# Performance work log

Measured on AMD Instinct MI355X. Metric: run time of the kernel, lower is better.

The kernel has to match this reference:

```python
import jax, jax.numpy as jnp
import numpy as np

B, L, D = 4, 2048, 256
H = 8
HD = D // H  # head_dim = 32


def setup_inputs() -> dict:
    key = jax.random.key(0)
    k1, k2, k3, k4 = jax.random.split(key, 4)
    x = jax.random.normal(k1, (B, L, D), dtype=jnp.float32)
    attn_bias = jax.random.normal(k2, (1, 1, L, L), dtype=jnp.float32)
    # Linear weights (stored as [in, out]; bias=False in the module)
    Wqkv = jax.random.normal(k3, (D, 3 * D), dtype=jnp.float32) * (D ** -0.5)
    Wout = jax.random.normal(k4, (D, D), dtype=jnp.float32) * (D ** -0.5)
    return {"x": x, "attn_bias": attn_bias, "Wqkv": Wqkv, "Wout": Wout}


def reference(x, attn_bias, Wqkv, Wout):
    scale = HD ** -0.5
    qkv = x @ Wqkv                                  # [B, L, 3D]
    q, k, v = jnp.split(qkv, 3, axis=-1)            # each [B, L, D]
    # b l (h d) -> b h l d
    def split_heads(t):
        return t.reshape(B, L, H, HD).transpose(0, 2, 1, 3)
    q, k, v = split_heads(q), split_heads(k), split_heads(v)
    scores = jnp.einsum('bhid,bhjd->bhij', q, k) * scale  # [B, H, L, L]
    scores = scores + attn_bias
    attn = jax.nn.softmax(scores, axis=-1)
    out = jnp.einsum('bhij,bhjd->bhid', attn, v)    # [B, H, L, HD]
    out = out.transpose(0, 2, 1, 3).reshape(B, L, D)
    return out @ Wout
```

## Files before the change

kernel.cpp:

```cpp
#include <hip/hip_runtime.h>
#include <hip/hip_bf16.h>
#include <math.h>

#define B 4
#define L 2048
#define D 256
#define H 8
#define HD 32
#define KVB 64
#define SCALE 0.17677669529663687f
#define LOG2E 1.4426950408889634f
#define QSCL (SCALE * LOG2E)

typedef __attribute__((ext_vector_type(8))) short short8;
typedef __attribute__((ext_vector_type(4))) short short4v;
typedef __attribute__((ext_vector_type(4))) float f32x4;

__device__ inline short f2bf(float x) {
  union { float f; unsigned u; } c; c.f = x;
  unsigned r = (c.u + 0x7FFFu + ((c.u >> 16) & 1u)) >> 16;
  return (short)r;
}
__device__ inline float bf2f(short s) {
  union { unsigned u; float f; } c;
  c.u = ((unsigned)(unsigned short)s) << 16;
  return c.f;
}

#define GLOAD_LDS16(gp, lp)                                                  \
  __builtin_amdgcn_global_load_lds(                                          \
      (const __attribute__((address_space(1))) unsigned*)(const void*)(gp),  \
      (__attribute__((address_space(3))) unsigned*)(void*)(lp), 16, 0, 0)


__global__ __launch_bounds__(256) void prep_xb(const float* __restrict__ x,
                                               short* __restrict__ xb) {
  int i = (blockIdx.x * 256 + threadIdx.x) * 8;
  f32x4 a = *reinterpret_cast<const f32x4*>(x + i);
  f32x4 b = *reinterpret_cast<const f32x4*>(x + i + 4);
  short8 o;
#pragma unroll
  for (int j = 0; j < 4; ++j) { o[j] = f2bf(a[j]); o[4 + j] = f2bf(b[j]); }
  *reinterpret_cast<short8*>(xb + i) = o;
}

__global__ __launch_bounds__(256) void prep_bias(const float* __restrict__ bias,
                                                 short* __restrict__ bp) {
  int base = (blockIdx.x * 256 + threadIdx.x) * 8;
  int q = base >> 11;
  int rem = base & 2047;
  int kvt = rem >> 6;
  int wi = rem & 63;
  int g = wi >> 4;
  int c0 = (wi & 15) >> 2;
  const float* src = bias + (long)q * L + kvt * 64 + c0 * 16 + g * 4;
  f32x4 b0 = *reinterpret_cast<const f32x4*>(src);
  f32x4 b1 = *reinterpret_cast<const f32x4*>(src + 16);
  short8 o;
#pragma unroll
  for (int j = 0; j < 4; ++j) { o[j] = f2bf(b0[j]); o[4 + j] = f2bf(b1[j]); }
  *reinterpret_cast<short8*>(bp + base) = o;
}

__global__ __launch_bounds__(256) void prep_wt(const float* __restrict__ w,
                                               short* __restrict__ wt, int N) {
  __shared__ short tile[32][33];
  int k0 = blockIdx.x * 32;
  int n0 = blockIdx.y * 32;
  int tx = threadIdx.x & 31, ty = threadIdx.x >> 5;
#pragma unroll
  for (int i = 0; i < 32; i += 8)
    tile[ty + i][tx] = f2bf(w[(k0 + ty + i) * N + n0 + tx]);
  __syncthreads();
#pragma unroll
  for (int i = 0; i < 32; i += 8)
    wt[(n0 + ty + i) * 256 + k0 + tx] = tile[tx][ty + i];
}

__global__ __launch_bounds__(64) void qkv_gemm(const short* __restrict__ xb,
                                               const short* __restrict__ wt,
                                               short* __restrict__ qb,
                                               short* __restrict__ kb,
                                               short* __restrict__ vt) {
  int bid = blockIdx.x;
  int mt = bid / 12, nt = bid % 12;
  int m0 = mt * 64, n0 = nt * 64;
  int l = threadIdx.x, ra = l & 15, g = l >> 4;

  f32x4 acc[4][4] = {};
  for (int k0 = 0; k0 < 256; k0 += 32) {
    int kk = k0 + g * 8;
    short8 bfr[4], afr[4];
#pragma unroll
    for (int nf = 0; nf < 4; ++nf)
      bfr[nf] = *reinterpret_cast<const short8*>(&wt[(n0 + nf * 16 + ra) * 256 + kk]);
#pragma unroll
    for (int mf = 0; mf < 4; ++mf)
      afr[mf] = *reinterpret_cast<const short8*>(&xb[(m0 + mf * 16 + ra) * 256 + kk]);
#pragma unroll
    for (int mf = 0; mf < 4; ++mf)
#pragma unroll
      for (int nf = 0; nf < 4; ++nf)
        acc[mf][nf] = __builtin_amdgcn_mfma_f32_16x16x32_bf16(afr[mf], bfr[nf], acc[mf][nf], 0, 0, 0);
  }

  int sec = n0 >> 8;
  float scl = (sec == 0) ? QSCL : 1.0f;
#pragma unroll
  for (int nf = 0; nf < 4; ++nf) {
    int n = n0 + nf * 16 + ra;
    int c = n & 255;
    int h = c >> 5, d = c & 31;
#pragma unroll
    for (int mf = 0; mf < 4; ++mf) {
#pragma unroll
      for (int r = 0; r < 4; ++r) {
        int mm = m0 + mf * 16 + g * 4 + r;
        int b = mm >> 11, lpos = mm & 2047;
        short val = f2bf(acc[mf][nf][r] * scl);
        if (sec == 2) vt[((b * H + h) * HD + d) * L + lpos] = val;
        else {
          short* dst = (sec == 0) ? qb : kb;
          dst[((b * H + h) * L + lpos) * HD + d] = val;
        }
      }
    }
  }
}

__global__ __launch_bounds__(512, 4) void attn_fwd(const short* __restrict__ qb,
                                                   const short* __restrict__ kb,
                                                   const short* __restrict__ vt,
                                                   const short* __restrict__ bp,
                                                   short* __restrict__ ob) {
  __shared__ short kvlds[2][8][512];

  int wid = threadIdx.x >> 6;
  int l = threadIdx.x & 63;
  int ra = l & 15, g = l >> 4;
  bool oddg = (g & 1);
  int x = blockIdx.x & 7;
  int y = (blockIdx.x >> 3) & 3;
  int qblk = blockIdx.x >> 5;
  int bh = x * 4 + y;
  int q0 = qblk * 128 + wid * 16;

  const short* kbase = kb + bh * (L * HD);
  const short* vbase = vt + bh * (HD * L);
  const short* bpbase = bp + (q0 + ra) * L + g * 16;

  short8 bq = *reinterpret_cast<const short8*>(qb + (bh * L + q0 + ra) * HD + g * 8);

  const short* gsrc0;
  int gstep;
  if (wid < 4) { gsrc0 = kbase + (16 * wid + ra) * HD + g * 8; gstep = KVB * HD; }
  else {
    int j = wid - 4;
    gsrc0 = vbase + ((j >> 1) * 16 + ra) * L + (j & 1) * 32 + g * 8;
    gstep = KVB;
  }

  f32x4 o0 = {}, o1 = {}, zf = {};
  float mrun = -1e30f, lsum = 0.f;
  short8 bbX[2], bbY[2];

  auto STAGE = [&](int buf, int t) {
    GLOAD_LDS16(gsrc0 + (size_t)t * gstep, &kvlds[buf][wid][0]);
  };
  auto BLOAD = [&](short8 (&bb)[2], int t) {
    const short* p = bpbase + t * KVB;
    bb[0] = *reinterpret_cast<const short8*>(p);
    bb[1] = *reinterpret_cast<const short8*>(p + 8);
  };

  auto TILE = [&](int buf, short8 (&bb)[2]) {
    const short* base = &kvlds[buf][0][0];
    short8 ak0 = *reinterpret_cast<const short8*>(base + 0 * 512 + l * 8);
    short8 ak1 = *reinterpret_cast<const short8*>(base + 1 * 512 + l * 8);
    short8 ak2 = *reinterpret_cast<const short8*>(base + 2 * 512 + l * 8);
    short8 ak3 = *reinterpret_cast<const short8*>(base + 3 * 512 + l * 8);
    short8 va0 = *reinterpret_cast<const short8*>(base + 4 * 512 + l * 8);
    short8 va1 = *reinterpret_cast<const short8*>(base + 5 * 512 + l * 8);
    short8 va2 = *reinterpret_cast<const short8*>(base + 6 * 512 + l * 8);
    short8 va3 = *reinterpret_cast<const short8*>(base + 7 * 512 + l * 8);

    f32x4 s0 = __builtin_amdgcn_mfma_f32_16x16x32_bf16(ak0, bq, zf, 0, 0, 0);
    f32x4 s1 = __builtin_amdgcn_mfma_f32_16x16x32_bf16(ak1, bq, zf, 0, 0, 0);
    f32x4 s2 = __builtin_amdgcn_mfma_f32_16x16x32_bf16(ak2, bq, zf, 0, 0, 0);
    f32x4 s3 = __builtin_amdgcn_mfma_f32_16x16x32_bf16(ak3, bq, zf, 0, 0, 0);

    float v[16];
#pragma unroll
    for (int r = 0; r < 4; ++r) {
      v[r]      = fmaf(bf2f(bb[0][r]),     LOG2E, s0[r]);
      v[4 + r]  = fmaf(bf2f(bb[0][4 + r]), LOG2E, s1[r]);
      v[8 + r]  = fmaf(bf2f(bb[1][r]),     LOG2E, s2[r]);
      v[12 + r] = fmaf(bf2f(bb[1][4 + r]), LOG2E, s3[r]);
    }
    float t0 = fmaxf(fmaxf(v[0], v[1]), v[2]);
    float t1 = fmaxf(fmaxf(v[3], v[4]), v[5]);
    float t2 = fmaxf(fmaxf(v[6], v[7]), v[8]);
    float t3 = fmaxf(fmaxf(v[9], v[10]), v[11]);
    float t4m = fmaxf(fmaxf(v[12], v[13]), v[14]);
    float pml = fmaxf(fmaxf(fmaxf(t0, t1), t2), fmaxf(fmaxf(t3, t4m), v[15]));

    if (!__all(pml <= mrun + 8.0f)) {
      float pm = fmaxf(pml, __shfl_xor(pml, 16));
      pm = fmaxf(pm, __shfl_xor(pm, 32));
      float mnew = fmaxf(mrun, pm);
      float ad = mrun - mnew, al;
      asm("v_exp_f32 %0, %1" : "=v"(al) : "v"(ad));
      lsum *= al;
#pragma unroll
      for (int r = 0; r < 4; ++r) { o0[r] *= al; o1[r] *= al; }
      mrun = mnew;
    }
    float m = mrun;
#pragma unroll
    for (int i = 0; i < 16; ++i) {
      float xv = v[i] - m;
      asm("v_exp_f32 %0, %1" : "=v"(v[i]) : "v"(xv));
    }
    float p01 = (v[0] + v[1]) + (v[2] + v[3]);
    float p23 = (v[4] + v[5]) + (v[6] + v[7]);
    float p45 = (v[8] + v[9]) + (v[10] + v[11]);
    float p67 = (v[12] + v[13]) + (v[14] + v[15]);
    lsum += (p01 + p23) + (p45 + p67);

#pragma unroll
    for (int ch = 0; ch < 2; ++ch) {
      const float* pc = v + ch * 8;
      unsigned w01, w23, w45, w67;
      asm("v_cvt_pk_bf16_f32 %0, %1, %2" : "=v"(w01) : "v"(pc[0]), "v"(pc[1]));
      asm("v_cvt_pk_bf16_f32 %0, %1, %2" : "=v"(w23) : "v"(pc[2]), "v"(pc[3]));
      asm("v_cvt_pk_bf16_f32 %0, %1, %2" : "=v"(w45) : "v"(pc[4]), "v"(pc[5]));
      asm("v_cvt_pk_bf16_f32 %0, %1, %2" : "=v"(w67) : "v"(pc[6]), "v"(pc[7]));
      asm("v_permlane32_swap_b32 %0, %1" : "+v"(w01), "+v"(w45));
      asm("v_permlane32_swap_b32 %0, %1" : "+v"(w23), "+v"(w67));
      unsigned z1 = oddg ? w01 : w45;
      unsigned z2 = oddg ? w23 : w67;
      unsigned y1 = (unsigned)__shfl_xor((int)z1, 16);
      unsigned y2 = (unsigned)__shfl_xor((int)z2, 16);
      union { unsigned u[4]; short8 s; } pb;
      pb.u[0] = oddg ? y1 : w01;
      pb.u[1] = oddg ? y2 : w23;
      pb.u[2] = oddg ? w45 : y1;
      pb.u[3] = oddg ? w67 : y2;
      o0 = __builtin_amdgcn_mfma_f32_16x16x32_bf16(ch ? va1 : va0, pb.s, o0, 0, 0, 0);
      o1 = __builtin_amdgcn_mfma_f32_16x16x32_bf16(ch ? va3 : va2, pb.s, o1, 0, 0, 0);
    }
  };

  STAGE(0, 0);
  BLOAD(bbX, 0);
  __syncthreads();
  for (int t = 0; t < 32; t += 2) {
    STAGE(1, t + 1);
    BLOAD(bbY, t + 1);
    TILE(0, bbX);
    __syncthreads();
    if (t + 2 < 32) { STAGE(0, t + 2); BLOAD(bbX, t + 2); }
    TILE(1, bbY);
    __syncthreads();
  }

  int b = bh >> 3, h = bh & 7;
  float ls = lsum;
  ls += __shfl_xor(ls, 16);
  ls += __shfl_xor(ls, 32);
  float inv = 1.0f / ls;
  int row = (b * L + q0 + ra) * D + h * HD;
  short4v w0, w1;
#pragma unroll
  for (int r = 0; r < 4; ++r) { w0[r] = f2bf(o0[r] * inv); w1[r] = f2bf(o1[r] * inv); }
  *reinterpret_cast<short4v*>(ob + row + g * 4) = w0;
  *reinterpret_cast<short4v*>(ob + row + 16 + g * 4) = w1;
}

__global__ __launch_bounds__(64) void out_gemm(const short* __restrict__ obuf,
                                               const short* __restrict__ wt,
                                               float* __restrict__ out) {
  int bid = blockIdx.x;
  int nt = bid & 3, mt = bid >> 2;
  int m0 = mt * 64, n0 = nt * 64;
  int l = threadIdx.x, ra = l & 15, g = l >> 4;

  f32x4 acc[4][4] = {};
  for (int k0 = 0; k0 < 256; k0 += 32) {
    int kk = k0 + g * 8;
    short8 bfr[4], afr[4];
#pragma unroll
    for (int nf = 0; nf < 4; ++nf)
      bfr[nf] = *reinterpret_cast<const short8*>(&wt[(n0 + nf * 16 + ra) * 256 + kk]);
#pragma unroll
    for (int mf = 0; mf < 4; ++mf)
      afr[mf] = *reinterpret_cast<const short8*>(&obuf[(m0 + mf * 16 + ra) * 256 + kk]);
#pragma unroll
    for (int mf = 0; mf < 4; ++mf)
#pragma unroll
      for (int nf = 0; nf < 4; ++nf)
        acc[mf][nf] = __builtin_amdgcn_mfma_f32_16x16x32_bf16(afr[mf], bfr[nf], acc[mf][nf], 0, 0, 0);
  }
#pragma unroll
  for (int mf = 0; mf < 4; ++mf)
#pragma unroll
    for (int nf = 0; nf < 4; ++nf)
#pragma unroll
      for (int r = 0; r < 4; ++r)
        out[(m0 + mf * 16 + g * 4 + r) * 256 + n0 + nf * 16 + ra] = acc[mf][nf][r];
}

extern "C" void kernel_launch(void* const* d_in, const int* in_sizes, int n_in,
                              void* d_out, int out_size, void* d_ws, size_t ws_size,
                              hipStream_t stream) {
  const float* x    = (const float*)d_in[0];
  const float* bias = (const float*)d_in[1];
  const float* wqkv = (const float*)d_in[2];
  const float* wout = (const float*)d_in[3];
  float* out = (float*)d_out;

  short* xb     = (short*)d_ws;
  short* qb     = xb + B * L * D;
  short* kb     = qb + B * L * D;
  short* vt     = kb + B * L * D;
  short* ob     = vt + B * L * D;
  short* wqkvT  = ob + B * L * D;
  short* woutT  = wqkvT + 768 * 256;
  short* biasp  = woutT + 256 * 256;

  prep_xb<<<dim3(1024), dim3(256), 0, stream>>>(x, xb);
  prep_bias<<<dim3(2048), dim3(256), 0, stream>>>(bias, biasp);
  prep_wt<<<dim3(8, 24), dim3(256), 0, stream>>>(wqkv, wqkvT, 768);
  prep_wt<<<dim3(8, 8), dim3(256), 0, stream>>>(wout, woutT, 256);
  qkv_gemm<<<dim3(1536), dim3(64), 0, stream>>>(xb, wqkvT, qb, kb, vt);
  attn_fwd<<<dim3(512), dim3(512), 0, stream>>>(qb, kb, vt, biasp, ob);
  out_gemm<<<dim3(512), dim3(64), 0, stream>>>(ob, woutT, out);
}
```

Before: 88.65 us.

## Split attention KV range across two wave halves and merge softmax partials

Each attention block now handles 64 query rows instead of 128, with two groups of four waves each processing half of the key/value sequence (split-K flash attention). Partial outputs, row sums and running maxima from the second half are exchanged through shared memory and merged with exp rescaling before writing. The grid doubles to 1024 blocks, the shared buffer doubles, and launch bounds request higher occupancy. This raises parallelism and shortens each block's serial KV loop, at the cost of an extra sync, a merge step, and loading each K/V tile once per half-block pair.

New measurement: 218.7 us. +146.7%, slower.

```diff
diff --git a/kernel.cpp b/kernel.cpp
--- a/kernel.cpp
+++ b/kernel.cpp
@@ -128,22 +128,24 @@
   }
 }
 
-__global__ __launch_bounds__(512, 4) void attn_fwd(const short* __restrict__ qb,
+__global__ __launch_bounds__(512, 8) void attn_fwd(const short* __restrict__ qb,
                                                    const short* __restrict__ kb,
                                                    const short* __restrict__ vt,
                                                    const short* __restrict__ bp,
                                                    short* __restrict__ ob) {
-  __shared__ short kvlds[2][8][512];
+  __shared__ short kvlds[2][2][8][512];
 
   int wid = threadIdx.x >> 6;
   int l = threadIdx.x & 63;
   int ra = l & 15, g = l >> 4;
   bool oddg = (g & 1);
-  int x = blockIdx.x & 7;
+  int swid = wid & 3, half = wid >> 2;
+  int kv0 = half * 1024;
+  int hgrp = blockIdx.x & 7;
   int y = (blockIdx.x >> 3) & 3;
   int qblk = blockIdx.x >> 5;
-  int bh = x * 4 + y;
-  int q0 = qblk * 128 + wid * 16;
+  int bh = hgrp * 4 + y;
+  int q0 = qblk * 64 + swid * 16;
 
   const short* kbase = kb + bh * (L * HD);
   const short* vbase = vt + bh * (HD * L);
@@ -151,12 +153,17 @@
 
   short8 bq = *reinterpret_cast<const short8*>(qb + (bh * L + q0 + ra) * HD + g * 8);
 
-  const short* gsrc0;
+  const short *gsrcA, *gsrcB;
   int gstep;
-  if (wid < 4) { gsrc0 = kbase + (16 * wid + ra) * HD + g * 8; gstep = KVB * HD; }
-  else {
-    int j = wid - 4;
-    gsrc0 = vbase + ((j >> 1) * 16 + ra) * L + (j & 1) * 32 + g * 8;
+  int sA = swid * 2, sB = sA + 1;
+  if (swid < 2) {
+    gsrcA = kbase + (size_t)(kv0 + 16 * sA + ra) * HD + g * 8;
+    gsrcB = kbase + (size_t)(kv0 + 16 * sB + ra) * HD + g * 8;
+    gstep = KVB * HD;
+  } else {
+    int jA = sA - 4, jB = sB - 4;
+    gsrcA = vbase + (size_t)((jA >> 1) * 16 + ra) * L + kv0 + (jA & 1) * 32 + g * 8;
+    gsrcB = vbase + (size_t)((jB >> 1) * 16 + ra) * L + kv0 + (jB & 1) * 32 + g * 8;
     gstep = KVB;
   }
 
@@ -165,16 +172,17 @@
   short8 bbX[2], bbY[2];
 
   auto STAGE = [&](int buf, int t) {
-    GLOAD_LDS16(gsrc0 + (size_t)t * gstep, &kvlds[buf][wid][0]);
+    GLOAD_LDS16(gsrcA + (size_t)t * gstep, &kvlds[buf][half][sA][0]);
+    GLOAD_LDS16(gsrcB + (size_t)t * gstep, &kvlds[buf][half][sB][0]);
   };
   auto BLOAD = [&](short8 (&bb)[2], int t) {
-    const short* p = bpbase + t * KVB;
+    const short* p = bpbase + (half * 16 + t) * KVB;
     bb[0] = *reinterpret_cast<const short8*>(p);
     bb[1] = *reinterpret_cast<const short8*>(p + 8);
   };
 
   auto TILE = [&](int buf, short8 (&bb)[2]) {
-    const short* base = &kvlds[buf][0][0];
+    const short* base = &kvlds[buf][half][0][0];
     short8 ak0 = *reinterpret_cast<const short8*>(base + 0 * 512 + l * 8);
     short8 ak1 = *reinterpret_cast<const short8*>(base + 1 * 512 + l * 8);
     short8 ak2 = *reinterpret_cast<const short8*>(base + 2 * 512 + l * 8);
@@ -254,27 +262,48 @@
   STAGE(0, 0);
   BLOAD(bbX, 0);
   __syncthreads();
-  for (int t = 0; t < 32; t += 2) {
+  for (int t = 0; t < 16; t += 2) {
     STAGE(1, t + 1);
     BLOAD(bbY, t + 1);
     TILE(0, bbX);
     __syncthreads();
-    if (t + 2 < 32) { STAGE(0, t + 2); BLOAD(bbX, t + 2); }
+    if (t + 2 < 16) { STAGE(0, t + 2); BLOAD(bbX, t + 2); }
     TILE(1, bbY);
     __syncthreads();
   }
 
-  int b = bh >> 3, h = bh & 7;
   float ls = lsum;
   ls += __shfl_xor(ls, 16);
   ls += __shfl_xor(ls, 32);
-  float inv = 1.0f / ls;
-  int row = (b * L + q0 + ra) * D + h * HD;
-  short4v w0, w1;
-#pragma unroll
-  for (int r = 0; r < 4; ++r) { w0[r] = f2bf(o0[r] * inv); w1[r] = f2bf(o1[r] * inv); }
-  *reinterpret_cast<short4v*>(ob + row + g * 4) = w0;
-  *reinterpret_cast<short4v*>(ob + row + 16 + g * 4) = w1;
+
+  float* xch = (float*)&kvlds[0][0][0][0];
+  float* slot = xch + (swid * 64 + l) * 10;
+  if (half == 1) {
+#pragma unroll
+    for (int r = 0; r < 4; ++r) { slot[r] = o0[r]; slot[4 + r] = o1[r]; }
+    slot[8] = ls;
+    slot[9] = mrun;
+  }
+  __syncthreads();
+  if (half == 0) {
+    float ls2 = slot[8], m2 = slot[9];
+    float mf = fmaxf(mrun, m2);
+    float d1 = mrun - mf, d2 = m2 - mf, a1, a2;
+    asm("v_exp_f32 %0, %1" : "=v"(a1) : "v"(d1));
+    asm("v_exp_f32 %0, %1" : "=v"(a2) : "v"(d2));
+    float lt = ls * a1 + ls2 * a2;
+    float inv = 1.0f / lt;
+    int b = bh >> 3, h = bh & 7;
+    int row = (b * L + q0 + ra) * D + h * HD;
+    short4v wo0, wo1;
+#pragma unroll
+    for (int r = 0; r < 4; ++r) {
+      wo0[r] = f2bf((o0[r] * a1 + slot[r] * a2) * inv);
+      wo1[r] = f2bf((o1[r] * a1 + slot[4 + r] * a2) * inv);
+    }
+    *reinterpret_cast<short4v*>(ob + row + g * 4) = wo0;
+    *reinterpret_cast<short4v*>(ob + row + 16 + g * 4) = wo1;
+  }
 }
 
 __global__ __launch_bounds__(64) void out_gemm(const short* __restrict__ obuf,
@@ -333,6 +362,6 @@
   prep_wt<<<dim3(8, 24), dim3(256), 0, stream>>>(wqkv, wqkvT, 768);
   prep_wt<<<dim3(8, 8), dim3(256), 0, stream>>>(wout, woutT, 256);
   qkv_gemm<<<dim3(1536), dim3(64), 0, stream>>>(xb, wqkvT, qb, kb, vt);
-  attn_fwd<<<dim3(512), dim3(512), 0, stream>>>(qb, kb, vt, biasp, ob);
+  attn_fwd<<<dim3(1024), dim3(512), 0, stream>>>(qb, kb, vt, biasp, ob);
   out_gemm<<<dim3(512), dim3(64), 0, stream>>>(ob, woutT, out);
 }
```
